# Kernel optimization log

Hardware: AMD Instinct MI355X
Metric: run time of the kernel (lower is better)

Reference implementation:

```python
import jax, jax.numpy as jnp
import numpy as np

B, T, S = 64, 128, 256
H = I = K = C = 2048
FLOAT_MIN = -100000.0


def setup_inputs() -> dict:
    key = jax.random.key(0)
    ks = jax.random.split(key, 10)
    s = 1.0 / np.sqrt(H)
    u = lambda k, shape: jax.random.uniform(k, shape, jnp.float32, -s, s)
    return dict(
        enc_keys=jax.random.normal(ks[0], (B, S, K), jnp.float32),
        enc_values=jax.random.normal(ks[1], (B, S, C), jnp.float32),
        enc_mask=jnp.ones((B, S, 1), jnp.float32),
        y=jax.random.normal(ks[2], (B, T, I), jnp.float32),
        W_attr=u(ks[3], (K, H)),
        V_attr=u(ks[4], (K,)),
        b_attr=u(ks[5], (K,)),
        # packed gate weights: rows [Wi; Wf; Wo; Wc] etc. (math-equivalent to 12 separate GEMMs)
        W_y=u(ks[6], (4 * H, I)),
        U_h=u(ks[7], (4 * H, H)),
        C_ctx=u(ks[8], (4 * H, C)),
        b=u(ks[9], (4 * H,)),
    )


def reference(enc_keys, enc_values, enc_mask, y, W_attr, V_attr, b_attr, W_y, U_h, C_ctx, b):
    Bq = y.shape[0]
    Hq = U_h.shape[1]

    def attend(h):
        q = h @ W_attr.T  # [B,K]
        e = jnp.sum(jnp.tanh(enc_keys + q[:, None, :] + b_attr) * V_attr, axis=2, keepdims=True)  # [B,S,1]
        e = enc_mask * e + (1.0 - enc_mask) * FLOAT_MIN
        scores = jax.nn.softmax(e, axis=1)  # [B,S,1]
        return jnp.sum(enc_values * scores, axis=1)  # [B,C]

    def step(carry, y_t):
        c, h = carry
        ctx = attend(h)
        gates = y_t @ W_y.T + h @ U_h.T + ctx @ C_ctx.T + b  # [B,4H]
        gi, gf, go, gc = jnp.split(gates, 4, axis=1)
        i = jax.nn.sigmoid(gi)
        f = jax.nn.sigmoid(gf)
        o = jax.nn.sigmoid(go)
        c_new = i * jnp.tanh(gc) + f * c
        h_new = o * jnp.tanh(c_new)
        return (c_new, h_new), (h_new, ctx)

    c0 = jnp.zeros((Bq, Hq), jnp.float32)
    h0 = jnp.zeros((Bq, Hq), jnp.float32)
    _, (hs, ctxs) = jax.lax.scan(step, (c0, h0), jnp.swapaxes(y, 0, 1))  # time-major scan
    # dropout is identity in eval mode
    return jnp.swapaxes(hs, 0, 1), jnp.swapaxes(ctxs, 0, 1)  # [B,T,H], [B,T,C]
```

## Files before the change

### kernel.cpp

```cpp
#include <hip/hip_runtime.h>

#define BB 64
#define TT 128
#define SS 256
#define HH 2048
#define G4H 8192
#define KSUM 6144
#define NKK_G 192
#define NKK_A 64

typedef __attribute__((ext_vector_type(4))) float f32x4;
typedef __attribute__((ext_vector_type(8))) _Float16 h16x8;
typedef __attribute__((ext_vector_type(4))) _Float16 h16x4;
typedef __attribute__((ext_vector_type(2))) _Float16 h16x2;

__device__ __forceinline__ f32x4 mfma16(h16x8 a, h16x8 b, f32x4 c) {
  return __builtin_amdgcn_mfma_f32_16x16x32_f16(a, b, c, 0, 0, 0);
}

__device__ __forceinline__ float fast_exp2(float x) { return __builtin_amdgcn_exp2f(x); }
__device__ __forceinline__ float fast_rcp(float x) { return __builtin_amdgcn_rcpf(x); }
__device__ __forceinline__ float fast_tanh(float x) {
  float e = fast_exp2(x * 2.8853900817779268f);
  return 1.0f - 2.0f * fast_rcp(e + 1.0f);
}
__device__ __forceinline__ float fast_sig(float x) {
  return fast_rcp(1.0f + fast_exp2(x * -1.4426950408889634f));
}


__global__ void cvt_f32_to_f16(const float* __restrict__ src, _Float16* __restrict__ dst, int n4) {
  int i = blockIdx.x * blockDim.x + threadIdx.x;
  int stride = gridDim.x * blockDim.x;
  for (; i < n4; i += stride) {
    f32x4 v = reinterpret_cast<const f32x4*>(src)[i];
    h16x4 h;
    h[0] = (_Float16)v[0]; h[1] = (_Float16)v[1];
    h[2] = (_Float16)v[2]; h[3] = (_Float16)v[3];
    reinterpret_cast<h16x4*>(dst)[i] = h;
  }
}

__global__ void cvt_keys(const float* __restrict__ src, const float* __restrict__ battr,
                         _Float16* __restrict__ dst, int n8) {
  int i = blockIdx.x * blockDim.x + threadIdx.x;
  int stride = gridDim.x * blockDim.x;
  for (; i < n8; i += stride) {
    size_t base = (size_t)i * 8;
    int k = (int)(base & (HH - 1));
    f32x4 v0 = *reinterpret_cast<const f32x4*>(src + base);
    f32x4 v1 = *reinterpret_cast<const f32x4*>(src + base + 4);
    f32x4 b0 = *reinterpret_cast<const f32x4*>(battr + k);
    f32x4 b1 = *reinterpret_cast<const f32x4*>(battr + k + 4);
    h16x8 o;
#pragma unroll
    for (int j = 0; j < 4; ++j) { o[j] = (_Float16)(v0[j] + b0[j]); o[4 + j] = (_Float16)(v1[j] + b1[j]); }
    *reinterpret_cast<h16x8*>(dst + base) = o;
  }
}

__global__ void transpose_y(const float* __restrict__ y, _Float16* __restrict__ yT) {
  int blk = blockIdx.x;
  int b = blk / TT, t = blk - b * TT;
  int i = threadIdx.x * 8;
  const float* s = y + ((size_t)b * TT + t) * HH + i;
  f32x4 v0 = *reinterpret_cast<const f32x4*>(s);
  f32x4 v1 = *reinterpret_cast<const f32x4*>(s + 4);
  h16x8 o;
#pragma unroll
  for (int j = 0; j < 4; ++j) { o[j] = (_Float16)v0[j]; o[4 + j] = (_Float16)v1[j]; }
  *reinterpret_cast<h16x8*>(yT + ((size_t)t * BB + b) * HH + i) = o;
}


__global__ void build_wgs(const float* __restrict__ U, const float* __restrict__ Cc,
                          const float* __restrict__ Wy, const float* __restrict__ bias,
                          _Float16* __restrict__ Wgs, float* __restrict__ bperm) {
  int ct = blockIdx.x;
  int kw = threadIdx.x >> 6, l = threadIdx.x & 63;
  int c = ct * 16 + (l & 15);
  int g = c & 3, hidx = c >> 2;
  size_t srow = ((size_t)g * HH + hidx) * HH;
  const float* seg[3] = {U + srow, Cc + srow, Wy + srow};
  int koff_lane = (l >> 4) * 8;
  for (int j = 0; j < 48; ++j) {
    int kk = j * 4 + kw;
    const float* s = seg[j >> 4] + (kk & 63) * 32 + koff_lane;
    f32x4 v0 = *reinterpret_cast<const f32x4*>(s);
    f32x4 v1 = *reinterpret_cast<const f32x4*>(s + 4);
    h16x8 o;
#pragma unroll
    for (int q = 0; q < 4; ++q) { o[q] = (_Float16)v0[q]; o[4 + q] = (_Float16)v1[q]; }
    *reinterpret_cast<h16x8*>(Wgs + (((size_t)ct * NKK_G + kk) * 64 + l) * 8) = o;
  }
  if (threadIdx.x < 16) bperm[c] = bias[g * HH + hidx];
}

__global__ void build_wahs(const float* __restrict__ W, _Float16* __restrict__ Wahs) {
  int ct = blockIdx.x;
  int kw = threadIdx.x >> 6, l = threadIdx.x & 63;
  int c = ct * 16 + (l & 15);
  const float* row = W + (size_t)c * HH + (l >> 4) * 8;
  for (int j = 0; j < 16; ++j) {
    int kk = j * 4 + kw;
    const float* s = row + kk * 32;
    f32x4 v0 = *reinterpret_cast<const f32x4*>(s);
    f32x4 v1 = *reinterpret_cast<const f32x4*>(s + 4);
    h16x8 o;
#pragma unroll
    for (int q = 0; q < 4; ++q) { o[q] = (_Float16)v0[q]; o[4 + q] = (_Float16)v1[q]; }
    *reinterpret_cast<h16x8*>(Wahs + (((size_t)ct * NKK_A + kk) * 64 + l) * 8) = o;
  }
}

__global__ void init_state(float* __restrict__ cst, _Float16* __restrict__ hA) {
  int i = blockIdx.x * blockDim.x + threadIdx.x;
  if (i < BB * HH) {
    cst[i] = 0.0f;
    hA[i] = (_Float16)0.0f;
  }
}


__global__ void qgemm(const _Float16* __restrict__ hIn, const _Float16* __restrict__ Wahs,
                      _Float16* __restrict__ qh) {
  int w = threadIdx.x >> 6, l = threadIdx.x & 63;
  int ct = blockIdx.x;
  const _Float16* bp = Wahs + (size_t)ct * (NKK_A * 512) + l * 8;
  const _Float16* ap = hIn + (size_t)(w * 16 + (l & 15)) * HH + (l >> 4) * 8;
  f32x4 acc0 = {0.f, 0.f, 0.f, 0.f}, acc1 = {0.f, 0.f, 0.f, 0.f};
  f32x4 acc2 = {0.f, 0.f, 0.f, 0.f}, acc3 = {0.f, 0.f, 0.f, 0.f};
#pragma unroll 2
  for (int kk = 0; kk < NKK_A; kk += 4) {
    h16x8 b0 = *reinterpret_cast<const h16x8*>(bp + (size_t)kk * 512);
    h16x8 b1 = *reinterpret_cast<const h16x8*>(bp + (size_t)(kk + 1) * 512);
    h16x8 b2 = *reinterpret_cast<const h16x8*>(bp + (size_t)(kk + 2) * 512);
    h16x8 b3 = *reinterpret_cast<const h16x8*>(bp + (size_t)(kk + 3) * 512);
    h16x8 a0 = *reinterpret_cast<const h16x8*>(ap + kk * 32);
    h16x8 a1 = *reinterpret_cast<const h16x8*>(ap + (kk + 1) * 32);
    h16x8 a2 = *reinterpret_cast<const h16x8*>(ap + (kk + 2) * 32);
    h16x8 a3 = *reinterpret_cast<const h16x8*>(ap + (kk + 3) * 32);
    acc0 = mfma16(a0, b0, acc0);
    acc1 = mfma16(a1, b1, acc1);
    acc2 = mfma16(a2, b2, acc2);
    acc3 = mfma16(a3, b3, acc3);
  }
  f32x4 acc = (acc0 + acc1) + (acc2 + acc3);
  int col = ct * 16 + (l & 15);
  int rbase = w * 16 + (l >> 4) * 4;
#pragma unroll
  for (int r = 0; r < 4; ++r)
    qh[(size_t)(rbase + r) * HH + col] = (_Float16)acc[r];
}

__global__ void energies(const _Float16* __restrict__ kh, const _Float16* __restrict__ qh,
                         const _Float16* __restrict__ vh, const float* __restrict__ mask,
                         float* __restrict__ e) {
  int b = blockIdx.x >> 5, sg = blockIdx.x & 31;
  int tid = threadIdx.x;
  int sl = tid >> 5, ln = tid & 31;
  int s = sg * 8 + sl;
  const _Float16* row = kh + (size_t)(b * SS + s) * HH + ln * 8;
  const _Float16* qrow = qh + (size_t)b * HH + ln * 8;
  const _Float16* vrow = vh + ln * 8;
  float acc = 0.0f;
#pragma unroll
  for (int ch = 0; ch < 8; ++ch) {
    h16x8 k8 = *reinterpret_cast<const h16x8*>(row + ch * 256);
    h16x8 q8 = *reinterpret_cast<const h16x8*>(qrow + ch * 256);
    h16x8 v8 = *reinterpret_cast<const h16x8*>(vrow + ch * 256);
    h16x8 x8 = k8 + q8;
#pragma unroll
    for (int j = 0; j < 8; ++j) {
      acc += (float)v8[j] * fast_tanh((float)x8[j]);
    }
  }
#pragma unroll
  for (int off = 16; off > 0; off >>= 1) acc += __shfl_xor(acc, off);
  if (ln == 0) {
    float m = mask[b * SS + s];
    e[b * SS + s] = m * acc + (1.0f - m) * (-100000.0f);
  }
}

__global__ void ctx_softmax(const float* __restrict__ e, const _Float16* __restrict__ evh,
                            _Float16* __restrict__ ctxh, float* __restrict__ outCtx, int t) {
  __shared__ float pb[SS];
  __shared__ float red[4];
  __shared__ float pf[4 * 512];
  int b = blockIdx.x >> 2, cq = blockIdx.x & 3;
  int tid = threadIdx.x;
  float p = fast_exp2(e[b * SS + tid] * 1.4426950408889634f);
  pb[tid] = p;
  float ws = p;
#pragma unroll
  for (int off = 32; off > 0; off >>= 1) ws += __shfl_xor(ws, off);
  if ((tid & 63) == 0) red[tid >> 6] = ws;
  __syncthreads();
  float rs = fast_rcp(red[0] + red[1] + red[2] + red[3]);
  int sg = tid >> 6, cs = tid & 63;
  const _Float16* base = evh + ((size_t)b * SS + sg * 64) * HH + cq * 512 + cs * 8;
  float acc[8] = {0.f, 0.f, 0.f, 0.f, 0.f, 0.f, 0.f, 0.f};
#pragma unroll 8
  for (int s = 0; s < 64; ++s) {
    h16x8 v = *reinterpret_cast<const h16x8*>(base + (size_t)s * HH);
    float ps = pb[sg * 64 + s];
#pragma unroll
    for (int j = 0; j < 8; ++j) acc[j] += ps * (float)v[j];
  }
#pragma unroll
  for (int j = 0; j < 8; ++j) pf[sg * 512 + cs * 8 + j] = acc[j];
  __syncthreads();
  {
    int c0 = tid * 2;
#pragma unroll
    for (int u = 0; u < 2; ++u) {
      int c = c0 + u;
      float sum = pf[c] + pf[512 + c] + pf[1024 + c] + pf[1536 + c];
      float val = sum * rs;
      outCtx[((size_t)b * TT + t) * HH + cq * 512 + c] = val;
      ctxh[(size_t)b * HH + cq * 512 + c] = (_Float16)val;
    }
  }
}

__global__ void __launch_bounds__(512)
gates_cell(const _Float16* __restrict__ hIn, const _Float16* __restrict__ ctxh,
           const _Float16* __restrict__ yT, const _Float16* __restrict__ Wgs,
           const float* __restrict__ bperm, float* __restrict__ cst,
           float* __restrict__ outH, _Float16* __restrict__ hOut, int t) {
  __shared__ float glds[64 * 33];
  int wq = threadIdx.x >> 6, l = threadIdx.x & 63;
  int mq = wq >> 1, cth = wq & 1;
  int cb = blockIdx.x;
  int ctg = cb * 2 + cth;
  const _Float16* bp = Wgs + (size_t)ctg * (NKK_G * 512) + l * 8;
  size_t arow = (size_t)(mq * 16 + (l & 15)) * HH + (l >> 4) * 8;
  f32x4 acc = {0.f, 0.f, 0.f, 0.f};
  {
    const _Float16* a = hIn + arow;
#pragma unroll 4
    for (int kk = 0; kk < 64; ++kk) {
      h16x8 bf = *reinterpret_cast<const h16x8*>(bp + (size_t)kk * 512);
      h16x8 af = *reinterpret_cast<const h16x8*>(a + kk * 32);
      acc = mfma16(af, bf, acc);
    }
  }
  {
    const _Float16* a = ctxh + arow;
    const _Float16* bp1 = bp + (size_t)64 * 512;
#pragma unroll 4
    for (int kk = 0; kk < 64; ++kk) {
      h16x8 bf = *reinterpret_cast<const h16x8*>(bp1 + (size_t)kk * 512);
      h16x8 af = *reinterpret_cast<const h16x8*>(a + kk * 32);
      acc = mfma16(af, bf, acc);
    }
  }
  {
    const _Float16* a = yT + (size_t)t * BB * HH + arow;
    const _Float16* bp2 = bp + (size_t)128 * 512;
#pragma unroll 4
    for (int kk = 0; kk < 64; ++kk) {
      h16x8 bf = *reinterpret_cast<const h16x8*>(bp2 + (size_t)kk * 512);
      h16x8 af = *reinterpret_cast<const h16x8*>(a + kk * 32);
      acc = mfma16(af, bf, acc);
    }
  }
  float bias = bperm[cb * 32 + cth * 16 + (l & 15)];
  int lcol = cth * 16 + (l & 15);
  int rb = mq * 16 + (l >> 4) * 4;
#pragma unroll
  for (int r = 0; r < 4; ++r)
    glds[(rb + r) * 33 + lcol] = acc[r] + bias;
  __syncthreads();
  int b = threadIdx.x >> 3, hl = threadIdx.x & 7;
  int h0 = cb * 8;
  float gi = glds[b * 33 + hl * 4 + 0];
  float gf = glds[b * 33 + hl * 4 + 1];
  float go = glds[b * 33 + hl * 4 + 2];
  float gc = glds[b * 33 + hl * 4 + 3];
  float ig = fast_sig(gi), fg = fast_sig(gf), og = fast_sig(go);
  int ci = b * HH + h0 + hl;
  float cN = ig * fast_tanh(gc) + fg * cst[ci];
  float hN = og * fast_tanh(cN);
  cst[ci] = cN;
  outH[((size_t)b * TT + t) * HH + h0 + hl] = hN;
  hOut[ci] = (_Float16)hN;
}


extern "C" void kernel_launch(void* const* d_in, const int* in_sizes, int n_in,
                              void* d_out, int out_size, void* d_ws, size_t ws_size,
                              hipStream_t stream) {
  const float* enc_keys   = (const float*)d_in[0];
  const float* enc_values = (const float*)d_in[1];
  const float* enc_mask   = (const float*)d_in[2];
  const float* y          = (const float*)d_in[3];
  const float* W_attr     = (const float*)d_in[4];
  const float* V_attr     = (const float*)d_in[5];
  const float* b_attr     = (const float*)d_in[6];
  const float* W_y        = (const float*)d_in[7];
  const float* U_h        = (const float*)d_in[8];
  const float* C_ctx      = (const float*)d_in[9];
  const float* bias       = (const float*)d_in[10];

  char* ws = (char*)d_ws;
  size_t off = 0;
  auto alloc = [&](size_t bytes) {
    void* p = ws + off;
    off += (bytes + 255) & ~(size_t)255;
    return p;
  };
  _Float16* kh   = (_Float16*)alloc((size_t)BB * SS * HH * 2);
  _Float16* evh  = (_Float16*)alloc((size_t)BB * SS * HH * 2);
  _Float16* Wahs = (_Float16*)alloc((size_t)HH * HH * 2);
  _Float16* Wgs  = (_Float16*)alloc((size_t)G4H * KSUM * 2);
  _Float16* yTh  = (_Float16*)alloc((size_t)BB * TT * HH * 2);
  _Float16* hA   = (_Float16*)alloc((size_t)BB * HH * 2);
  _Float16* hB   = (_Float16*)alloc((size_t)BB * HH * 2);
  _Float16* ctxh = (_Float16*)alloc((size_t)BB * HH * 2);
  _Float16* qh   = (_Float16*)alloc((size_t)BB * HH * 2);
  _Float16* vhb  = (_Float16*)alloc((size_t)HH * 2);
  float* e       = (float*)alloc((size_t)BB * SS * 4);
  float* cst     = (float*)alloc((size_t)BB * HH * 4);
  float* bperm   = (float*)alloc((size_t)G4H * 4);
  (void)ws_size; (void)in_sizes; (void)n_in; (void)out_size;

  float* outH = (float*)d_out;
  float* outCtx = outH + (size_t)BB * TT * HH;

  cvt_keys<<<2048, 256, 0, stream>>>(enc_keys, b_attr, kh, BB * SS * HH / 8);
  cvt_f32_to_f16<<<2048, 256, 0, stream>>>(enc_values, evh, BB * SS * HH / 4);
  cvt_f32_to_f16<<<2, 256, 0, stream>>>(V_attr, vhb, HH / 4);
  build_wahs<<<HH / 16, 256, 0, stream>>>(W_attr, Wahs);
  build_wgs<<<G4H / 16, 256, 0, stream>>>(U_h, C_ctx, W_y, bias, Wgs, bperm);
  transpose_y<<<BB * TT, 256, 0, stream>>>(y, yTh);
  init_state<<<(BB * HH + 255) / 256, 256, 0, stream>>>(cst, hA);

  for (int t = 0; t < TT; ++t) {
    const _Float16* hIn = (t & 1) ? hB : hA;
    _Float16* hOut      = (t & 1) ? hA : hB;
    qgemm<<<HH / 16, 256, 0, stream>>>(hIn, Wahs, qh);
    energies<<<BB * SS / 8, 256, 0, stream>>>(kh, qh, vhb, enc_mask, e);
    ctx_softmax<<<BB * 4, 256, 0, stream>>>(e, evh, ctxh, outCtx, t);
    gates_cell<<<G4H / 32, 512, 0, stream>>>(hIn, ctxh, yTh, Wgs, bperm, cst, outH, hOut, t);
  }
}
```

Measured before the change: 12.69 ms.

## Hoist input projection out of recurrence and stage gate weights via LDS

Moves the y_t @ W_y^T term and the bias out of the per-step gates kernel into a single up-front batched GEMM over all timesteps. The result is stored as fp16 in a Gy buffer that each step reads as its accumulator initial value. This removes a third of the per-step weight streaming. The gates kernel also now double-buffers weight tiles into LDS with global_load_lds, so the two row-group waves no longer re-fetch the same weights. The costs are an extra 128MB workspace buffer and an extra fp16 rounding of the input projection.

```diff
diff --git a/kernel.cpp b/kernel.cpp
--- a/kernel.cpp
+++ b/kernel.cpp
@@ -5,14 +5,17 @@
 #define SS 256
 #define HH 2048
 #define G4H 8192
-#define KSUM 6144
-#define NKK_G 192
+#define KSUM 4096
+#define NKK_G 128
 #define NKK_A 64
 
 typedef __attribute__((ext_vector_type(4))) float f32x4;
 typedef __attribute__((ext_vector_type(8))) _Float16 h16x8;
 typedef __attribute__((ext_vector_type(4))) _Float16 h16x4;
 typedef __attribute__((ext_vector_type(2))) _Float16 h16x2;
+
+typedef __attribute__((address_space(1))) const void GV;
+typedef __attribute__((address_space(3))) void SV;
 
 __device__ __forceinline__ f32x4 mfma16(h16x8 a, h16x8 b, f32x4 c) {
   return __builtin_amdgcn_mfma_f32_16x16x32_f16(a, b, c, 0, 0, 0);
@@ -74,16 +77,16 @@
 
 
 __global__ void build_wgs(const float* __restrict__ U, const float* __restrict__ Cc,
-                          const float* __restrict__ Wy, const float* __restrict__ bias,
+                          const float* __restrict__ bias,
                           _Float16* __restrict__ Wgs, float* __restrict__ bperm) {
   int ct = blockIdx.x;
   int kw = threadIdx.x >> 6, l = threadIdx.x & 63;
   int c = ct * 16 + (l & 15);
   int g = c & 3, hidx = c >> 2;
   size_t srow = ((size_t)g * HH + hidx) * HH;
-  const float* seg[3] = {U + srow, Cc + srow, Wy + srow};
+  const float* seg[2] = {U + srow, Cc + srow};
   int koff_lane = (l >> 4) * 8;
-  for (int j = 0; j < 48; ++j) {
+  for (int j = 0; j < 32; ++j) {
     int kk = j * 4 + kw;
     const float* s = seg[j >> 4] + (kk & 63) * 32 + koff_lane;
     f32x4 v0 = *reinterpret_cast<const f32x4*>(s);
@@ -94,6 +97,24 @@
     *reinterpret_cast<h16x8*>(Wgs + (((size_t)ct * NKK_G + kk) * 64 + l) * 8) = o;
   }
   if (threadIdx.x < 16) bperm[c] = bias[g * HH + hidx];
+}
+
+__global__ void build_wys(const float* __restrict__ Wy, _Float16* __restrict__ Wys) {
+  int ct = blockIdx.x;
+  int kw = threadIdx.x >> 6, l = threadIdx.x & 63;
+  int c = ct * 16 + (l & 15);
+  int g = c & 3, hidx = c >> 2;
+  const float* row = Wy + ((size_t)g * HH + hidx) * HH + (l >> 4) * 8;
+  for (int j = 0; j < 16; ++j) {
+    int kk = j * 4 + kw;
+    const float* s = row + kk * 32;
+    f32x4 v0 = *reinterpret_cast<const f32x4*>(s);
+    f32x4 v1 = *reinterpret_cast<const f32x4*>(s + 4);
+    h16x8 o;
+#pragma unroll
+    for (int q = 0; q < 4; ++q) { o[q] = (_Float16)v0[q]; o[4 + q] = (_Float16)v1[q]; }
+    *reinterpret_cast<h16x8*>(Wys + (((size_t)ct * NKK_A + kk) * 64 + l) * 8) = o;
+  }
 }
 
 __global__ void build_wahs(const float* __restrict__ W, _Float16* __restrict__ Wahs) {
@@ -110,6 +131,49 @@
 #pragma unroll
     for (int q = 0; q < 4; ++q) { o[q] = (_Float16)v0[q]; o[4 + q] = (_Float16)v1[q]; }
     *reinterpret_cast<h16x8*>(Wahs + (((size_t)ct * NKK_A + kk) * 64 + l) * 8) = o;
+  }
+}
+
+__global__ void __launch_bounds__(512)
+gy_gemm(const _Float16* __restrict__ yT, const _Float16* __restrict__ Wys,
+        const float* __restrict__ bperm, _Float16* __restrict__ Gy) {
+  int tid = threadIdx.x;
+  int w = tid >> 6, l = tid & 63;
+  int wr = w >> 2, wc = w & 3;
+  int br = blockIdx.x & 63, bc = blockIdx.x >> 6;
+  const _Float16* abase = yT + ((size_t)(br * 128 + wr * 64 + (l & 15))) * HH + (l >> 4) * 8;
+  const _Float16* bbase = Wys + ((size_t)(bc * 16 + wc * 4) * NKK_A) * 512 + l * 8;
+  f32x4 acc[4][4] = {};
+#pragma unroll 1
+  for (int kk = 0; kk < NKK_A; ++kk) {
+    h16x8 a0 = *reinterpret_cast<const h16x8*>(abase + (size_t)0 * 16 * HH + kk * 32);
+    h16x8 a1 = *reinterpret_cast<const h16x8*>(abase + (size_t)1 * 16 * HH + kk * 32);
+    h16x8 a2 = *reinterpret_cast<const h16x8*>(abase + (size_t)2 * 16 * HH + kk * 32);
+    h16x8 a3 = *reinterpret_cast<const h16x8*>(abase + (size_t)3 * 16 * HH + kk * 32);
+    h16x8 b0 = *reinterpret_cast<const h16x8*>(bbase + ((size_t)0 * NKK_A + kk) * 512);
+    h16x8 b1 = *reinterpret_cast<const h16x8*>(bbase + ((size_t)1 * NKK_A + kk) * 512);
+    h16x8 b2 = *reinterpret_cast<const h16x8*>(bbase + ((size_t)2 * NKK_A + kk) * 512);
+    h16x8 b3 = *reinterpret_cast<const h16x8*>(bbase + ((size_t)3 * NKK_A + kk) * 512);
+    acc[0][0] = mfma16(a0, b0, acc[0][0]); acc[0][1] = mfma16(a0, b1, acc[0][1]);
+    acc[0][2] = mfma16(a0, b2, acc[0][2]); acc[0][3] = mfma16(a0, b3, acc[0][3]);
+    acc[1][0] = mfma16(a1, b0, acc[1][0]); acc[1][1] = mfma16(a1, b1, acc[1][1]);
+    acc[1][2] = mfma16(a1, b2, acc[1][2]); acc[1][3] = mfma16(a1, b3, acc[1][3]);
+    acc[2][0] = mfma16(a2, b0, acc[2][0]); acc[2][1] = mfma16(a2, b1, acc[2][1]);
+    acc[2][2] = mfma16(a2, b2, acc[2][2]); acc[2][3] = mfma16(a2, b3, acc[2][3]);
+    acc[3][0] = mfma16(a3, b0, acc[3][0]); acc[3][1] = mfma16(a3, b1, acc[3][1]);
+    acc[3][2] = mfma16(a3, b2, acc[3][2]); acc[3][3] = mfma16(a3, b3, acc[3][3]);
+  }
+#pragma unroll
+  for (int q = 0; q < 4; ++q) {
+#pragma unroll
+    for (int cc = 0; cc < 4; ++cc) {
+      int col = (bc * 16 + wc * 4 + cc) * 16 + (l & 15);
+      float bv = bperm[col];
+      int r0 = br * 128 + wr * 64 + q * 16 + (l >> 4) * 4;
+#pragma unroll
+      for (int r = 0; r < 4; ++r)
+        Gy[(size_t)(r0 + r) * G4H + col] = (_Float16)(acc[q][cc][r] + bv);
+    }
   }
 }
 
@@ -226,54 +290,63 @@
 
 __global__ void __launch_bounds__(512)
 gates_cell(const _Float16* __restrict__ hIn, const _Float16* __restrict__ ctxh,
-           const _Float16* __restrict__ yT, const _Float16* __restrict__ Wgs,
-           const float* __restrict__ bperm, float* __restrict__ cst,
-           float* __restrict__ outH, _Float16* __restrict__ hOut, int t) {
+           const _Float16* __restrict__ Gy, const _Float16* __restrict__ Wgs,
+           float* __restrict__ cst, float* __restrict__ outH,
+           _Float16* __restrict__ hOut, int t) {
+  __shared__ _Float16 Bsm[2][2][16][512];
   __shared__ float glds[64 * 33];
-  int wq = threadIdx.x >> 6, l = threadIdx.x & 63;
-  int mq = wq >> 1, cth = wq & 1;
+  int tid = threadIdx.x;
+  int w = tid >> 6, l = tid & 63;
+  int mq = w >> 1, cth = w & 1;
   int cb = blockIdx.x;
-  int ctg = cb * 2 + cth;
-  const _Float16* bp = Wgs + (size_t)ctg * (NKK_G * 512) + l * 8;
+
+  int col = cb * 32 + cth * 16 + (l & 15);
+  int rb = mq * 16 + (l >> 4) * 4;
+  f32x4 acc;
+  {
+    const _Float16* gy = Gy + ((size_t)(t * 64 + rb)) * G4H + col;
+    acc[0] = (float)gy[0];
+    acc[1] = (float)gy[(size_t)G4H];
+    acc[2] = (float)gy[(size_t)2 * G4H];
+    acc[3] = (float)gy[(size_t)3 * G4H];
+  }
+
   size_t arow = (size_t)(mq * 16 + (l & 15)) * HH + (l >> 4) * 8;
-  f32x4 acc = {0.f, 0.f, 0.f, 0.f};
-  {
-    const _Float16* a = hIn + arow;
-#pragma unroll 4
-    for (int kk = 0; kk < 64; ++kk) {
-      h16x8 bf = *reinterpret_cast<const h16x8*>(bp + (size_t)kk * 512);
-      h16x8 af = *reinterpret_cast<const h16x8*>(a + kk * 32);
+
+  auto STAGE = [&](int buf, int c) {
+#pragma unroll
+    for (int u = 0; u < 4; ++u) {
+      int idx = w * 4 + u;
+      int ctgl = idx >> 4, slot = idx & 15;
+      const _Float16* g = Wgs + (((size_t)(cb * 2 + ctgl) * NKK_G + c * 16 + slot) * 64 + l) * 8;
+      __builtin_amdgcn_global_load_lds((GV*)g, (SV*)&Bsm[buf][ctgl][slot][0], 16, 0, 0);
+    }
+  };
+
+  STAGE(0, 0);
+  __syncthreads();
+  int buf = 0;
+#pragma unroll 1
+  for (int c = 0; c < 8; ++c) {
+    if (c < 7) STAGE(buf ^ 1, c + 1);
+    const _Float16* a = (c < 4 ? hIn : ctxh) + arow;
+    int kloc = (c & 3) * 16;
+#pragma unroll
+    for (int s = 0; s < 16; ++s) {
+      h16x8 bf = *reinterpret_cast<const h16x8*>(&Bsm[buf][cth][s][l * 8]);
+      h16x8 af = *reinterpret_cast<const h16x8*>(a + (kloc + s) * 32);
       acc = mfma16(af, bf, acc);
     }
-  }
-  {
-    const _Float16* a = ctxh + arow;
-    const _Float16* bp1 = bp + (size_t)64 * 512;
-#pragma unroll 4
-    for (int kk = 0; kk < 64; ++kk) {
-      h16x8 bf = *reinterpret_cast<const h16x8*>(bp1 + (size_t)kk * 512);
-      h16x8 af = *reinterpret_cast<const h16x8*>(a + kk * 32);
-      acc = mfma16(af, bf, acc);
-    }
-  }
-  {
-    const _Float16* a = yT + (size_t)t * BB * HH + arow;
-    const _Float16* bp2 = bp + (size_t)128 * 512;
-#pragma unroll 4
-    for (int kk = 0; kk < 64; ++kk) {
-      h16x8 bf = *reinterpret_cast<const h16x8*>(bp2 + (size_t)kk * 512);
-      h16x8 af = *reinterpret_cast<const h16x8*>(a + kk * 32);
-      acc = mfma16(af, bf, acc);
-    }
-  }
-  float bias = bperm[cb * 32 + cth * 16 + (l & 15)];
+    __syncthreads();
+    buf ^= 1;
+  }
+
   int lcol = cth * 16 + (l & 15);
-  int rb = mq * 16 + (l >> 4) * 4;
 #pragma unroll
   for (int r = 0; r < 4; ++r)
-    glds[(rb + r) * 33 + lcol] = acc[r] + bias;
+    glds[(rb + r) * 33 + lcol] = acc[r];
   __syncthreads();
-  int b = threadIdx.x >> 3, hl = threadIdx.x & 7;
+  int b = tid >> 3, hl = tid & 7;
   int h0 = cb * 8;
   float gi = glds[b * 33 + hl * 4 + 0];
   float gf = glds[b * 33 + hl * 4 + 1];
@@ -315,6 +388,8 @@
   _Float16* evh  = (_Float16*)alloc((size_t)BB * SS * HH * 2);
   _Float16* Wahs = (_Float16*)alloc((size_t)HH * HH * 2);
   _Float16* Wgs  = (_Float16*)alloc((size_t)G4H * KSUM * 2);
+  _Float16* Wys  = (_Float16*)alloc((size_t)G4H * HH * 2);
+  _Float16* Gy   = (_Float16*)alloc((size_t)BB * TT * G4H * 2);
   _Float16* yTh  = (_Float16*)alloc((size_t)BB * TT * HH * 2);
   _Float16* hA   = (_Float16*)alloc((size_t)BB * HH * 2);
   _Float16* hB   = (_Float16*)alloc((size_t)BB * HH * 2);
@@ -333,8 +408,10 @@
   cvt_f32_to_f16<<<2048, 256, 0, stream>>>(enc_values, evh, BB * SS * HH / 4);
   cvt_f32_to_f16<<<2, 256, 0, stream>>>(V_attr, vhb, HH / 4);
   build_wahs<<<HH / 16, 256, 0, stream>>>(W_attr, Wahs);
-  build_wgs<<<G4H / 16, 256, 0, stream>>>(U_h, C_ctx, W_y, bias, Wgs, bperm);
+  build_wgs<<<G4H / 16, 256, 0, stream>>>(U_h, C_ctx, bias, Wgs, bperm);
+  build_wys<<<G4H / 16, 256, 0, stream>>>(W_y, Wys);
   transpose_y<<<BB * TT, 256, 0, stream>>>(y, yTh);
+  gy_gemm<<<2048, 512, 0, stream>>>(yTh, Wys, bperm, Gy);
   init_state<<<(BB * HH + 255) / 256, 256, 0, stream>>>(cst, hA);
 
   for (int t = 0; t < TT; ++t) {
@@ -343,6 +420,6 @@
     qgemm<<<HH / 16, 256, 0, stream>>>(hIn, Wahs, qh);
     energies<<<BB * SS / 8, 256, 0, stream>>>(kh, qh, vhb, enc_mask, e);
     ctx_softmax<<<BB * 4, 256, 0, stream>>>(e, evh, ctxh, outCtx, t);
-    gates_cell<<<G4H / 32, 512, 0, stream>>>(hIn, ctxh, yTh, Wgs, bperm, cst, outH, hOut, t);
-  }
-}
+    gates_cell<<<G4H / 32, 512, 0, stream>>>(hIn, ctxh, Gy, Wgs, cst, outH, hOut, t);
+  }
+}
```

New measurement: 10.55 ms. 16.9% less time.
